# Performance work log

Hardware: AMD Instinct MI355X
Metric: run time of the kernel (lower is better)

Reference implementation:

```python
import jax, jax.numpy as jnp
import numpy as np

D_MODEL = 1024
N_HEADS = 16
HEAD_DIM = D_MODEL // N_HEADS
EPS = 1e-5


def layer_norm(x, g, b):
    mu = jnp.mean(x, axis=-1, keepdims=True)
    var = jnp.mean(jnp.square(x - mu), axis=-1, keepdims=True)
    return (x - mu) * jax.lax.rsqrt(var + EPS) * g + b


def setup_inputs() -> dict:
    key = jax.random.key(0)
    ks = jax.random.split(key, 16)
    B, S, D = 4, 2048, D_MODEL
    s = 1.0 / np.sqrt(D)
    inp = {
        "query": jax.random.normal(ks[0], (B, S, D), jnp.float32),
        "key": jax.random.normal(ks[1], (B, S, D), jnp.float32),
        "value": jax.random.normal(ks[2], (B, S, D), jnp.float32),
        "Wq": jax.random.normal(ks[3], (D, D), jnp.float32) * s,
        "bq": jnp.zeros((D,), jnp.float32),
        "Wk": jax.random.normal(ks[4], (D, D), jnp.float32) * s,
        "bk": jnp.zeros((D,), jnp.float32),
        "Wv": jax.random.normal(ks[5], (D, D), jnp.float32) * s,
        "bv": jnp.zeros((D,), jnp.float32),
        "Wo": jax.random.normal(ks[6], (D, D), jnp.float32) * s,
        "bo": jnp.zeros((D,), jnp.float32),
        "Wg": jax.random.normal(ks[7], (D, 1), jnp.float32) * s,
        "ln_q_g": jnp.ones((D,), jnp.float32),
        "ln_q_b": jnp.zeros((D,), jnp.float32),
        "ln_kv_g": jnp.ones((D,), jnp.float32),
        "ln_kv_b": jnp.zeros((D,), jnp.float32),
        "ln_o_g": jnp.ones((D,), jnp.float32),
        "ln_o_b": jnp.zeros((D,), jnp.float32),
    }
    return inp


def reference(query, key, value, Wq, bq, Wk, bk, Wv, bv, Wo, bo, Wg,
              ln_q_g, ln_q_b, ln_kv_g, ln_kv_b, ln_o_g, ln_o_b):
    B, S, D = query.shape
    H, Hd = N_HEADS, HEAD_DIM
    scale = Hd ** -0.5
    # pre-norms (note: key and value share norm_kv params, as in source)
    qn = layer_norm(query, ln_q_g, ln_q_b)
    kn = layer_norm(key, ln_kv_g, ln_kv_b)
    vn = layer_norm(value, ln_kv_g, ln_kv_b)
    q = (qn @ Wq + bq).reshape(B, S, H, Hd)
    k = (kn @ Wk + bk).reshape(B, S, H, Hd)
    v = (vn @ Wv + bv).reshape(B, S, H, Hd)
    scores = jnp.einsum("bqhd,bkhd->bhqk", q, k) * scale  # [B,H,S,S]
    attn = jax.nn.softmax(scores, axis=-1)  # temperature = 1.0
    out = jnp.einsum("bhqk,bkhd->bqhd", attn, v).reshape(B, S, D)
    out = out @ Wo + bo
    gate = jax.nn.sigmoid(qn @ Wg)  # [B,S,1]
    out = gate * out
    out = layer_norm(out, ln_o_g, ln_o_b)
    return out
```

## Files before the change

kernel.cpp:

```cpp
#include <hip/hip_runtime.h>

#define DEV static __device__ __forceinline__

typedef unsigned short u16;
typedef __attribute__((ext_vector_type(4))) float f32x4;
typedef __attribute__((ext_vector_type(8))) __bf16 bf16x8;
typedef __attribute__((ext_vector_type(8))) unsigned short us8;
typedef __attribute__((ext_vector_type(4))) unsigned short us4;

DEV u16 f2b(float f){
  unsigned u = __float_as_uint(f);
  u += 0x7fffu + ((u >> 16) & 1u);
  return (u16)(u >> 16);
}

DEV void gl_lds16(const void* g, void* l){
  __builtin_amdgcn_global_load_lds(
      (__attribute__((address_space(1))) void*)(void*)g,
      (__attribute__((address_space(3))) void*)l, 16, 0, 0);
}

__global__ __launch_bounds__(256) void wtrans(const float* __restrict__ W,
                                              u16* __restrict__ Wt){
  __shared__ float tile[32][33];
  const int tx = threadIdx.x, ty = threadIdx.y;
  const int x  = blockIdx.x*32 + tx;
  const int y0 = blockIdx.y*32 + ty;
  #pragma unroll
  for (int i=0;i<32;i+=8) tile[ty+i][tx] = W[(size_t)(y0+i)*1024 + x];
  __syncthreads();
  const int xo  = blockIdx.y*32 + tx;
  const int yo0 = blockIdx.x*32 + ty;
  #pragma unroll
  for (int i=0;i<32;i+=8) Wt[(size_t)(yo0+i)*1024 + xo] = f2b(tile[tx][ty+i]);
}

__global__ __launch_bounds__(256) void ln_in(
    const float* __restrict__ src,
    const float* __restrict__ gp, const float* __restrict__ bp,
    const float* __restrict__ Wg,
    u16* __restrict__ dst, float* __restrict__ gate)
{
  __shared__ float red[8];
  const int row = blockIdx.x, tid = threadIdx.x;
  const int lane = tid & 63, w = tid >> 6;

  const float4 x = ((const float4*)(src + (size_t)row*1024))[tid];
  float s  = x.x + x.y + x.z + x.w;
  float ss = x.x*x.x + x.y*x.y + x.z*x.z + x.w*x.w;
  #pragma unroll
  for (int o=32;o;o>>=1){ s += __shfl_down(s,o); ss += __shfl_down(ss,o); }
  if (lane==0){ red[w] = s; red[4+w] = ss; }
  __syncthreads();
  s  = red[0]+red[1]+red[2]+red[3];
  ss = red[4]+red[5]+red[6]+red[7];
  const float mu   = s * (1.0f/1024.0f);
  const float rstd = rsqrtf(ss*(1.0f/1024.0f) - mu*mu + 1e-5f);
  const float4 gg = ((const float4*)gp)[tid];
  const float4 bb = ((const float4*)bp)[tid];
  const float y0 = (x.x-mu)*rstd*gg.x + bb.x;
  const float y1 = (x.y-mu)*rstd*gg.y + bb.y;
  const float y2 = (x.z-mu)*rstd*gg.z + bb.z;
  const float y3 = (x.w-mu)*rstd*gg.w + bb.w;
  us4 o4 = { f2b(y0), f2b(y1), f2b(y2), f2b(y3) };
  ((us4*)(dst + (size_t)row*1024))[tid] = o4;

  if (Wg){
    const float4 wg = ((const float4*)Wg)[tid];
    float gd = y0*wg.x + y1*wg.y + y2*wg.z + y3*wg.w;
    __syncthreads();
    #pragma unroll
    for (int o=32;o;o>>=1) gd += __shfl_down(gd,o);
    if (lane==0) red[w] = gd;
    __syncthreads();
    if (tid==0){
      const float dsum = red[0]+red[1]+red[2]+red[3];
      gate[row] = 1.0f / (1.0f + __expf(-dsum));
    }
  }
}

template<int OUTMODE>
__global__ __launch_bounds__(256) void gemm_bt(
    const u16* __restrict__ A, const u16* __restrict__ Bt,
    const float* __restrict__ bias, const float* __restrict__ gate,
    void* __restrict__ Cout, int M, int N, int K)
{
  constexpr int BK = 32;
  __shared__ __align__(16) u16 As[128*BK];
  __shared__ __align__(16) u16 Bs[128*BK];
  const int tid = threadIdx.x, lane = tid & 63, w = tid >> 6;
  const int wr = w >> 1, wc = w & 1;
  const int bm = blockIdx.y * 128, bn = blockIdx.x * 128;

  f32x4 acc[4][4];
  #pragma unroll
  for (int m=0;m<4;m++)
    #pragma unroll
    for (int n=0;n<4;n++) acc[m][n] = (f32x4){0.f,0.f,0.f,0.f};

  const int r_in = lane >> 2, kc_in = (lane & 3) * 8;
  const u16* Ag = A  + (size_t)(bm + w*16 + r_in)*K + kc_in;
  const u16* Bg = Bt + (size_t)(bn + w*16 + r_in)*K + kc_in;
  u16* AsW = As + (w*16)*BK;
  u16* BsW = Bs + (w*16)*BK;

  for (int kt=0; kt<K; kt+=BK){
    gl_lds16(Ag + kt,              AsW);
    gl_lds16(Ag + (size_t)64*K+kt, AsW + 64*BK);
    gl_lds16(Bg + kt,              BsW);
    gl_lds16(Bg + (size_t)64*K+kt, BsW + 64*BK);
    __syncthreads();
    bf16x8 af[4], bfr[4];
    #pragma unroll
    for (int m=0;m<4;m++)
      af[m] = *(const bf16x8*)(As + (wr*64 + m*16 + (lane&15))*BK + (lane>>4)*8);
    #pragma unroll
    for (int n=0;n<4;n++)
      bfr[n] = *(const bf16x8*)(Bs + (wc*64 + n*16 + (lane&15))*BK + (lane>>4)*8);
    #pragma unroll
    for (int m=0;m<4;m++)
      #pragma unroll
      for (int n=0;n<4;n++)
        acc[m][n] = __builtin_amdgcn_mfma_f32_16x16x32_bf16(af[m], bfr[n], acc[m][n], 0, 0, 0);
    __syncthreads();
  }

  #pragma unroll
  for (int m=0;m<4;m++){
    const int row0 = bm + wr*64 + m*16 + ((lane>>4)<<2);
    #pragma unroll
    for (int n=0;n<4;n++){
      const int col = bn + wc*64 + n*16 + (lane&15);
      const float bv = bias[col];
      if (OUTMODE == 2){
        const int bidx = row0 >> 11, srow = row0 & 2047;
        const int h = col >> 6, dcol = col & 63;
        us4 pk = { f2b(acc[m][n][0]+bv), f2b(acc[m][n][1]+bv),
                   f2b(acc[m][n][2]+bv), f2b(acc[m][n][3]+bv) };
        *(us4*)((u16*)Cout + ((size_t)(bidx*16+h)*64 + dcol)*2048 + srow) = pk;
      } else {
        #pragma unroll
        for (int r=0;r<4;r++){
          const float val = acc[m][n][r] + bv;
          if (OUTMODE == 1)
            ((float*)Cout)[(size_t)(row0+r)*N + col] = val * gate[row0+r];
          else
            ((u16*)Cout)[(size_t)(row0+r)*N + col] = f2b(val);
        }
      }
    }
  }
}

__global__ __launch_bounds__(256) void attn(
    const u16* __restrict__ qg, const u16* __restrict__ kg,
    const u16* __restrict__ vt, u16* __restrict__ og)
{
  constexpr int S = 2048, D = 1024;
  __shared__ __align__(16) u16 Ks[2][64][72];
  __shared__ __align__(16) u16 Vs[2][64][72];
  __shared__ __align__(16) u16 Pl[4][16][72];
  const int bh = blockIdx.y, b = bh >> 4, h = bh & 15;
  const int q0 = blockIdx.x * 64;
  const int tid = threadIdx.x, lane = tid & 63, w = tid >> 6;
  const size_t kbase  = (size_t)b * S * D + h * 64;
  const size_t vtbase = (size_t)(b*16 + h) * 64 * S;
  const int rr = tid >> 3, cc = (tid & 7) * 8;

  const int qr = q0 + w*16 + (lane & 15);
  const bf16x8 aq0 = *(const bf16x8*)(qg + kbase + (size_t)qr*D +      (lane>>4)*8);
  const bf16x8 aq1 = *(const bf16x8*)(qg + kbase + (size_t)qr*D + 32 + (lane>>4)*8);

  const us8 one_u = {0x3F80,0x3F80,0x3F80,0x3F80,0x3F80,0x3F80,0x3F80,0x3F80};
  const bf16x8 vones = *(const bf16x8*)&one_u;

  f32x4 acc[4];
  #pragma unroll
  for (int n=0;n<4;n++) acc[n] = (f32x4){0.f,0.f,0.f,0.f};
  f32x4 accl = (f32x4){0.f,0.f,0.f,0.f};
  float mrun[4];
  #pragma unroll
  for (int r=0;r<4;r++) mrun[r] = -1e30f;

  us8 kr0, kr1, vr0, vr1;
  #define LOADT(t) do { \
    kr0 = *(const us8*)(kg + kbase + (size_t)((t)+rr)*D + cc);      \
    kr1 = *(const us8*)(kg + kbase + (size_t)((t)+32+rr)*D + cc);   \
    vr0 = *(const us8*)(vt + vtbase + (size_t)rr*S + (t) + cc);     \
    vr1 = *(const us8*)(vt + vtbase + (size_t)(32+rr)*S + (t) + cc);\
  } while(0)
  #define STORET(bi) do { \
    *(us8*)&Ks[bi][rr][cc]    = kr0; *(us8*)&Ks[bi][32+rr][cc] = kr1; \
    *(us8*)&Vs[bi][rr][cc]    = vr0; *(us8*)&Vs[bi][32+rr][cc] = vr1; \
  } while(0)

  LOADT(0); STORET(0); LOADT(64);
  __syncthreads();

  for (int t=0; t<S; t+=64){
    const int cur = (t>>6) & 1;

    f32x4 s[4];
    #pragma unroll
    for (int sc=0;sc<4;sc++){
      bf16x8 bk0 = *(const bf16x8*)(&Ks[cur][sc*16 + (lane&15)][     (lane>>4)*8]);
      bf16x8 bk1 = *(const bf16x8*)(&Ks[cur][sc*16 + (lane&15)][32 + (lane>>4)*8]);
      f32x4 z = (f32x4){0.f,0.f,0.f,0.f};
      z = __builtin_amdgcn_mfma_f32_16x16x32_bf16(aq0, bk0, z, 0,0,0);
      z = __builtin_amdgcn_mfma_f32_16x16x32_bf16(aq1, bk1, z, 0,0,0);
      s[sc] = z * 0.125f;
    }

    float mxr[4];
    #pragma unroll
    for (int r=0;r<4;r++)
      mxr[r] = fmaxf(fmaxf(s[0][r],s[1][r]), fmaxf(s[2][r],s[3][r]));
    #pragma unroll
    for (int o=1;o<16;o<<=1)
      #pragma unroll
      for (int r=0;r<4;r++) mxr[r] = fmaxf(mxr[r], __shfl_xor(mxr[r], o));

    bool need = false;
    #pragma unroll
    for (int r=0;r<4;r++) need |= (mxr[r] > mrun[r] + 8.0f);
    if (__any(need)){
      #pragma unroll
      for (int r=0;r<4;r++){
        const float mn = fmaxf(mrun[r], mxr[r]);
        const float fac = __expf(mrun[r]-mn);
        mrun[r] = mn; accl[r] *= fac;
        #pragma unroll
        for (int n=0;n<4;n++) acc[n][r] *= fac;
      }
    }

    #pragma unroll
    for (int sc=0;sc<4;sc++)
      #pragma unroll
      for (int r=0;r<4;r++)
        Pl[w][(lane>>4)*4 + r][sc*16 + (lane&15)] = f2b(__expf(s[sc][r] - mrun[r]));

    #pragma unroll
    for (int kc=0;kc<2;kc++){
      bf16x8 ap = *(const bf16x8*)(&Pl[w][lane&15][kc*32 + (lane>>4)*8]);
      accl = __builtin_amdgcn_mfma_f32_16x16x32_bf16(ap, vones, accl, 0,0,0);
      #pragma unroll
      for (int n=0;n<4;n++){
        bf16x8 bv = *(const bf16x8*)(&Vs[cur][n*16 + (lane&15)][kc*32 + (lane>>4)*8]);
        acc[n] = __builtin_amdgcn_mfma_f32_16x16x32_bf16(ap, bv, acc[n], 0,0,0);
      }
    }

    __syncthreads();
    if (t + 64 < S){
      STORET(cur^1);
      if (t + 128 < S) LOADT(t+128);
      __syncthreads();
    }
  }

  #pragma unroll
  for (int r=0;r<4;r++){
    const float inv = 1.0f / accl[r];
    const int row = q0 + w*16 + ((lane>>4)<<2) + r;
    #pragma unroll
    for (int n=0;n<4;n++)
      og[(size_t)(b*S + row)*D + h*64 + n*16 + (lane&15)] = f2b(acc[n][r] * inv);
  }
  #undef LOADT
  #undef STORET
}

__global__ __launch_bounds__(256) void ln_out(
    const float* __restrict__ proj, const float* __restrict__ g,
    const float* __restrict__ b, float* __restrict__ out)
{
  __shared__ float red[8];
  const int row = blockIdx.x, tid = threadIdx.x;
  const int lane = tid & 63, w = tid >> 6;
  const float4 x = ((const float4*)(proj + (size_t)row*1024))[tid];
  float s  = x.x + x.y + x.z + x.w;
  float ss = x.x*x.x + x.y*x.y + x.z*x.z + x.w*x.w;
  #pragma unroll
  for (int o=32;o;o>>=1){ s += __shfl_down(s,o); ss += __shfl_down(ss,o); }
  if (lane==0){ red[w] = s; red[4+w] = ss; }
  __syncthreads();
  s  = red[0]+red[1]+red[2]+red[3];
  ss = red[4]+red[5]+red[6]+red[7];
  const float mu   = s * (1.0f/1024.0f);
  const float rstd = rsqrtf(ss*(1.0f/1024.0f) - mu*mu + 1e-5f);
  const float4 gg = ((const float4*)g)[tid];
  const float4 bb = ((const float4*)b)[tid];
  float4 o4;
  o4.x = (x.x-mu)*rstd*gg.x + bb.x;
  o4.y = (x.y-mu)*rstd*gg.y + bb.y;
  o4.z = (x.z-mu)*rstd*gg.z + bb.z;
  o4.w = (x.w-mu)*rstd*gg.w + bb.w;
  ((float4*)(out + (size_t)row*1024))[tid] = o4;
}

extern "C" void kernel_launch(void* const* d_in, const int* in_sizes, int n_in,
                              void* d_out, int out_size, void* d_ws, size_t ws_size,
                              hipStream_t stream) {
  const float* query = (const float*)d_in[0];
  const float* key_  = (const float*)d_in[1];
  const float* value = (const float*)d_in[2];
  const float* Wq = (const float*)d_in[3];
  const float* bq = (const float*)d_in[4];
  const float* Wk = (const float*)d_in[5];
  const float* bk = (const float*)d_in[6];
  const float* Wv = (const float*)d_in[7];
  const float* bv = (const float*)d_in[8];
  const float* Wo = (const float*)d_in[9];
  const float* bo = (const float*)d_in[10];
  const float* Wg = (const float*)d_in[11];
  const float* ln_q_g  = (const float*)d_in[12];
  const float* ln_q_b  = (const float*)d_in[13];
  const float* ln_kv_g = (const float*)d_in[14];
  const float* ln_kv_b = (const float*)d_in[15];
  const float* ln_o_g  = (const float*)d_in[16];
  const float* ln_o_b  = (const float*)d_in[17];

  constexpr int M = 8192, D = 1024;
  constexpr size_t WSZ = (size_t)D*D*2;
  constexpr size_t TSZ = (size_t)M*D*2;

  char* ws = (char*)d_ws;
  u16* WqT = (u16*)(ws + 0*WSZ);
  u16* WkT = (u16*)(ws + 1*WSZ);
  u16* WvT = (u16*)(ws + 2*WSZ);
  u16* WoT = (u16*)(ws + 3*WSZ);
  float* gate = (float*)(ws + 4*WSZ);
  u16* n_buf  = (u16*)(ws + 4*WSZ + 65536);
  u16* qb     = (u16*)(ws + 4*WSZ + 65536 + TSZ);
  u16* kb = (u16*)d_out;
  u16* vtb = (u16*)((char*)d_out + TSZ);
  float* proj = (float*)d_out;

  dim3 tb(32, 8);
  wtrans<<<dim3(32,32), tb, 0, stream>>>(Wq, WqT);
  wtrans<<<dim3(32,32), tb, 0, stream>>>(Wk, WkT);
  wtrans<<<dim3(32,32), tb, 0, stream>>>(Wv, WvT);
  wtrans<<<dim3(32,32), tb, 0, stream>>>(Wo, WoT);

  ln_in<<<M, 256, 0, stream>>>(query, ln_q_g, ln_q_b, Wg, n_buf, gate);
  gemm_bt<0><<<dim3(8,64), 256, 0, stream>>>(n_buf, WqT, bq, nullptr, qb, M, D, D);
  ln_in<<<M, 256, 0, stream>>>(key_, ln_kv_g, ln_kv_b, nullptr, n_buf, nullptr);
  gemm_bt<0><<<dim3(8,64), 256, 0, stream>>>(n_buf, WkT, bk, nullptr, kb, M, D, D);
  ln_in<<<M, 256, 0, stream>>>(value, ln_kv_g, ln_kv_b, nullptr, n_buf, nullptr);
  gemm_bt<2><<<dim3(8,64), 256, 0, stream>>>(n_buf, WvT, bv, nullptr, vtb, M, D, D);

  attn<<<dim3(32,64), 256, 0, stream>>>(qb, kb, vtb, n_buf);

  gemm_bt<1><<<dim3(8,64), 256, 0, stream>>>(n_buf, WoT, bo, gate, proj, M, D, D);
  ln_out<<<M, 256, 0, stream>>>(proj, ln_o_g, ln_o_b, (float*)d_out);
}
```

Before: 514.0 us.

## Rewrite attention with 32x32 MFMA, transposed scores, and register-resident P

```diff
diff --git a/kernel.cpp b/kernel.cpp
--- a/kernel.cpp
+++ b/kernel.cpp
@@ -3,7 +3,9 @@
 #define DEV static __device__ __forceinline__
 
 typedef unsigned short u16;
+typedef unsigned int u32;
 typedef __attribute__((ext_vector_type(4))) float f32x4;
+typedef __attribute__((ext_vector_type(16))) float f32x16;
 typedef __attribute__((ext_vector_type(8))) __bf16 bf16x8;
 typedef __attribute__((ext_vector_type(8))) unsigned short us8;
 typedef __attribute__((ext_vector_type(4))) unsigned short us4;
@@ -18,6 +20,15 @@
   __builtin_amdgcn_global_load_lds(
       (__attribute__((address_space(1))) void*)(void*)g,
       (__attribute__((address_space(3))) void*)l, 16, 0, 0);
+}
+
+DEV u32 pkbf(float lo, float hi){
+  u32 r;
+  asm("v_cvt_pk_bf16_f32 %0, %1, %2" : "=v"(r) : "v"(lo), "v"(hi));
+  return r;
+}
+DEV void pswap(u32 &a, u32 &b){
+  asm("v_permlane32_swap_b32 %0, %1" : "+v"(a), "+v"(b));
 }
 
 __global__ __launch_bounds__(256) void wtrans(const float* __restrict__ W,
@@ -84,7 +95,7 @@
 __global__ __launch_bounds__(256) void gemm_bt(
     const u16* __restrict__ A, const u16* __restrict__ Bt,
     const float* __restrict__ bias, const float* __restrict__ gate,
-    void* __restrict__ Cout, int M, int N, int K)
+    void* __restrict__ Cout, int M, int N, int K, float scale)
 {
   constexpr int BK = 32;
   __shared__ __align__(16) u16 As[128*BK];
@@ -142,7 +153,7 @@
       } else {
         #pragma unroll
         for (int r=0;r<4;r++){
-          const float val = acc[m][n][r] + bv;
+          const float val = (acc[m][n][r] + bv) * scale;
           if (OUTMODE == 1)
             ((float*)Cout)[(size_t)(row0+r)*N + col] = val * gate[row0+r];
           else
@@ -158,30 +169,25 @@
     const u16* __restrict__ vt, u16* __restrict__ og)
 {
   constexpr int S = 2048, D = 1024;
+  constexpr float L2E = 1.4426950408889634f;
   __shared__ __align__(16) u16 Ks[2][64][72];
   __shared__ __align__(16) u16 Vs[2][64][72];
-  __shared__ __align__(16) u16 Pl[4][16][72];
   const int bh = blockIdx.y, b = bh >> 4, h = bh & 15;
-  const int q0 = blockIdx.x * 64;
+  const int q0 = blockIdx.x * 128;
   const int tid = threadIdx.x, lane = tid & 63, w = tid >> 6;
+  const int l31 = lane & 31, hi = lane >> 5;
   const size_t kbase  = (size_t)b * S * D + h * 64;
-  const size_t vtbase = (size_t)(b*16 + h) * 64 * S;
+  const size_t vtbase = (size_t)bh * 64 * S;
   const int rr = tid >> 3, cc = (tid & 7) * 8;
 
-  const int qr = q0 + w*16 + (lane & 15);
-  const bf16x8 aq0 = *(const bf16x8*)(qg + kbase + (size_t)qr*D +      (lane>>4)*8);
-  const bf16x8 aq1 = *(const bf16x8*)(qg + kbase + (size_t)qr*D + 32 + (lane>>4)*8);
-
-  const us8 one_u = {0x3F80,0x3F80,0x3F80,0x3F80,0x3F80,0x3F80,0x3F80,0x3F80};
-  const bf16x8 vones = *(const bf16x8*)&one_u;
-
-  f32x4 acc[4];
-  #pragma unroll
-  for (int n=0;n<4;n++) acc[n] = (f32x4){0.f,0.f,0.f,0.f};
-  f32x4 accl = (f32x4){0.f,0.f,0.f,0.f};
-  float mrun[4];
-  #pragma unroll
-  for (int r=0;r<4;r++) mrun[r] = -1e30f;
+  const int qrow = q0 + w*32 + l31;
+  bf16x8 qf[4];
+  #pragma unroll
+  for (int c=0;c<4;c++)
+    qf[c] = *(const bf16x8*)(qg + kbase + (size_t)qrow*D + c*16 + hi*8);
+
+  f32x16 o0 = (f32x16)(0.f), o1 = (f32x16)(0.f);
+  float mrun = -1e30f, lsum = 0.f;
 
   us8 kr0, kr1, vr0, vr1;
   #define LOADT(t) do { \
@@ -201,55 +207,85 @@
   for (int t=0; t<S; t+=64){
     const int cur = (t>>6) & 1;
 
-    f32x4 s[4];
-    #pragma unroll
-    for (int sc=0;sc<4;sc++){
-      bf16x8 bk0 = *(const bf16x8*)(&Ks[cur][sc*16 + (lane&15)][     (lane>>4)*8]);
-      bf16x8 bk1 = *(const bf16x8*)(&Ks[cur][sc*16 + (lane&15)][32 + (lane>>4)*8]);
-      f32x4 z = (f32x4){0.f,0.f,0.f,0.f};
-      z = __builtin_amdgcn_mfma_f32_16x16x32_bf16(aq0, bk0, z, 0,0,0);
-      z = __builtin_amdgcn_mfma_f32_16x16x32_bf16(aq1, bk1, z, 0,0,0);
-      s[sc] = z * 0.125f;
-    }
-
-    float mxr[4];
-    #pragma unroll
-    for (int r=0;r<4;r++)
-      mxr[r] = fmaxf(fmaxf(s[0][r],s[1][r]), fmaxf(s[2][r],s[3][r]));
-    #pragma unroll
-    for (int o=1;o<16;o<<=1)
-      #pragma unroll
-      for (int r=0;r<4;r++) mxr[r] = fmaxf(mxr[r], __shfl_xor(mxr[r], o));
-
-    bool need = false;
-    #pragma unroll
-    for (int r=0;r<4;r++) need |= (mxr[r] > mrun[r] + 8.0f);
-    if (__any(need)){
-      #pragma unroll
-      for (int r=0;r<4;r++){
-        const float mn = fmaxf(mrun[r], mxr[r]);
-        const float fac = __expf(mrun[r]-mn);
-        mrun[r] = mn; accl[r] *= fac;
+    f32x16 s0 = (f32x16)(0.f), s1 = (f32x16)(0.f);
+    #pragma unroll
+    for (int c=0;c<4;c++){
+      bf16x8 kf0 = *(const bf16x8*)(&Ks[cur][l31]   [c*16 + hi*8]);
+      bf16x8 kf1 = *(const bf16x8*)(&Ks[cur][32+l31][c*16 + hi*8]);
+      s0 = __builtin_amdgcn_mfma_f32_32x32x16_bf16(kf0, qf[c], s0, 0,0,0);
+      s1 = __builtin_amdgcn_mfma_f32_32x32x16_bf16(kf1, qf[c], s1, 0,0,0);
+    }
+
+    float mx;
+    {
+      f32x16 mv;
+      #pragma unroll
+      for (int i=0;i<16;i++) mv[i] = fmaxf(s0[i], s1[i]);
+      #pragma unroll
+      for (int st=8; st; st>>=1)
         #pragma unroll
-        for (int n=0;n<4;n++) acc[n][r] *= fac;
+        for (int i=0;i<st;i++) mv[i] = fmaxf(mv[i], mv[i+st]);
+      mx = fmaxf(mv[0], __shfl_xor(mv[0], 32));
+    }
+
+    if (__any(mx > mrun + 8.0f)){
+      const float newm = fmaxf(mrun, mx);
+      const float fac = exp2f((mrun - newm) * L2E);
+      lsum *= fac;
+      #pragma unroll
+      for (int j=0;j<16;j++){
+        const int q_r = (j&3) + 8*(j>>2) + 4*hi;
+        const float fr = __shfl(fac, q_r);
+        o0[j] *= fr; o1[j] *= fr;
       }
-    }
-
-    #pragma unroll
-    for (int sc=0;sc<4;sc++)
-      #pragma unroll
-      for (int r=0;r<4;r++)
-        Pl[w][(lane>>4)*4 + r][sc*16 + (lane&15)] = f2b(__expf(s[sc][r] - mrun[r]));
-
-    #pragma unroll
-    for (int kc=0;kc<2;kc++){
-      bf16x8 ap = *(const bf16x8*)(&Pl[w][lane&15][kc*32 + (lane>>4)*8]);
-      accl = __builtin_amdgcn_mfma_f32_16x16x32_bf16(ap, vones, accl, 0,0,0);
-      #pragma unroll
-      for (int n=0;n<4;n++){
-        bf16x8 bv = *(const bf16x8*)(&Vs[cur][n*16 + (lane&15)][kc*32 + (lane>>4)*8]);
-        acc[n] = __builtin_amdgcn_mfma_f32_16x16x32_bf16(ap, bv, acc[n], 0,0,0);
-      }
+      mrun = newm;
+    }
+
+    const float ml = mrun * L2E;
+    f32x16 e0, e1;
+    #pragma unroll
+    for (int i=0;i<16;i++) e0[i] = exp2f(__builtin_fmaf(s0[i], L2E, -ml));
+    #pragma unroll
+    for (int i=0;i<16;i++) e1[i] = exp2f(__builtin_fmaf(s1[i], L2E, -ml));
+
+    {
+      f32x16 sv;
+      #pragma unroll
+      for (int i=0;i<16;i++) sv[i] = e0[i] + e1[i];
+      #pragma unroll
+      for (int st=8; st; st>>=1)
+        #pragma unroll
+        for (int i=0;i<st;i++) sv[i] += sv[i+st];
+      lsum += sv[0] + __shfl_xor(sv[0], 32);
+    }
+
+    union { u32 w[4]; bf16x8 v; } pa[4];
+    {
+      u32 a,bm_;
+      a = pkbf(e0[0], e0[1]);  bm_ = pkbf(e0[4], e0[5]);  pswap(a,bm_);
+      pa[0].w[0]=a; pa[0].w[2]=bm_;
+      a = pkbf(e0[2], e0[3]);  bm_ = pkbf(e0[6], e0[7]);  pswap(a,bm_);
+      pa[0].w[1]=a; pa[0].w[3]=bm_;
+      a = pkbf(e0[8], e0[9]);  bm_ = pkbf(e0[12],e0[13]); pswap(a,bm_);
+      pa[1].w[0]=a; pa[1].w[2]=bm_;
+      a = pkbf(e0[10],e0[11]); bm_ = pkbf(e0[14],e0[15]); pswap(a,bm_);
+      pa[1].w[1]=a; pa[1].w[3]=bm_;
+      a = pkbf(e1[0], e1[1]);  bm_ = pkbf(e1[4], e1[5]);  pswap(a,bm_);
+      pa[2].w[0]=a; pa[2].w[2]=bm_;
+      a = pkbf(e1[2], e1[3]);  bm_ = pkbf(e1[6], e1[7]);  pswap(a,bm_);
+      pa[2].w[1]=a; pa[2].w[3]=bm_;
+      a = pkbf(e1[8], e1[9]);  bm_ = pkbf(e1[12],e1[13]); pswap(a,bm_);
+      pa[3].w[0]=a; pa[3].w[2]=bm_;
+      a = pkbf(e1[10],e1[11]); bm_ = pkbf(e1[14],e1[15]); pswap(a,bm_);
+      pa[3].w[1]=a; pa[3].w[3]=bm_;
+    }
+
+    #pragma unroll
+    for (int c=0;c<4;c++){
+      bf16x8 vf0 = *(const bf16x8*)(&Vs[cur][l31]   [c*16 + hi*8]);
+      bf16x8 vf1 = *(const bf16x8*)(&Vs[cur][32+l31][c*16 + hi*8]);
+      o0 = __builtin_amdgcn_mfma_f32_32x32x16_bf16(pa[c].v, vf0, o0, 0,0,0);
+      o1 = __builtin_amdgcn_mfma_f32_32x32x16_bf16(pa[c].v, vf1, o1, 0,0,0);
     }
 
     __syncthreads();
@@ -260,13 +296,14 @@
     }
   }
 
-  #pragma unroll
-  for (int r=0;r<4;r++){
-    const float inv = 1.0f / accl[r];
-    const int row = q0 + w*16 + ((lane>>4)<<2) + r;
-    #pragma unroll
-    for (int n=0;n<4;n++)
-      og[(size_t)(b*S + row)*D + h*64 + n*16 + (lane&15)] = f2b(acc[n][r] * inv);
+  const float inv = 1.0f / lsum;
+  #pragma unroll
+  for (int j=0;j<16;j++){
+    const int q_r = (j&3) + 8*(j>>2) + 4*hi;
+    const float iv = __shfl(inv, q_r);
+    const size_t rowb = (size_t)(b*S + q0 + w*32 + q_r)*D + h*64;
+    og[rowb +      l31] = f2b(o0[j] * iv);
+    og[rowb + 32 + l31] = f2b(o1[j] * iv);
   }
   #undef LOADT
   #undef STORET
@@ -345,14 +382,14 @@
   wtrans<<<dim3(32,32), tb, 0, stream>>>(Wo, WoT);
 
   ln_in<<<M, 256, 0, stream>>>(query, ln_q_g, ln_q_b, Wg, n_buf, gate);
-  gemm_bt<0><<<dim3(8,64), 256, 0, stream>>>(n_buf, WqT, bq, nullptr, qb, M, D, D);
+  gemm_bt<0><<<dim3(8,64), 256, 0, stream>>>(n_buf, WqT, bq, nullptr, qb, M, D, D, 0.125f);
   ln_in<<<M, 256, 0, stream>>>(key_, ln_kv_g, ln_kv_b, nullptr, n_buf, nullptr);
-  gemm_bt<0><<<dim3(8,64), 256, 0, stream>>>(n_buf, WkT, bk, nullptr, kb, M, D, D);
+  gemm_bt<0><<<dim3(8,64), 256, 0, stream>>>(n_buf, WkT, bk, nullptr, kb, M, D, D, 1.0f);
   ln_in<<<M, 256, 0, stream>>>(value, ln_kv_g, ln_kv_b, nullptr, n_buf, nullptr);
-  gemm_bt<2><<<dim3(8,64), 256, 0, stream>>>(n_buf, WvT, bv, nullptr, vtb, M, D, D);
-
-  attn<<<dim3(32,64), 256, 0, stream>>>(qb, kb, vtb, n_buf);
-
-  gemm_bt<1><<<dim3(8,64), 256, 0, stream>>>(n_buf, WoT, bo, gate, proj, M, D, D);
+  gemm_bt<2><<<dim3(8,64), 256, 0, stream>>>(n_buf, WvT, bv, nullptr, vtb, M, D, D, 1.0f);
+
+  attn<<<dim3(16,64), 256, 0, stream>>>(qb, kb, vtb, n_buf);
+
+  gemm_bt<1><<<dim3(8,64), 256, 0, stream>>>(n_buf, WoT, bo, gate, proj, M, D, D, 1.0f);
   ln_out<<<M, 256, 0, stream>>>(proj, ln_o_g, ln_o_b, (float*)d_out);
 }
```

Result: faster. 463.3 us (-9.9%).
